# Performance work log

Hardware: AMD Instinct MI355X
Metric: run time of the kernel (lower is better)

## Reference

```python
import jax, jax.numpy as jnp
import numpy as np

B, C, H, W = 16, 256, 64, 64
K, D = 1024, 256  # codebook_dim, feature_dim (== channel)


def setup_inputs() -> dict:
    key = jax.random.key(0)
    k1, k2, k3, k4 = jax.random.split(key, 4)
    return {
        "x": jax.random.normal(k1, (B, C, H, W), dtype=jnp.float32),
        "conv_w": jax.random.normal(k2, (C, C), dtype=jnp.float32) * 0.05,
        "conv_b": jax.random.normal(k3, (C,), dtype=jnp.float32) * 0.05,
        "codebook": jax.random.normal(k4, (K, D), dtype=jnp.float32),
    }


def reference(x, conv_w, conv_b, codebook):
    # 1x1 conv: pure channel mix
    q = jnp.einsum("bchw,oc->bohw", x, conv_w) + conv_b[None, :, None, None]
    # NCHW -> NHWC -> flatten to [N, D]
    feat = jnp.transpose(q, (0, 2, 3, 1))  # [B,H,W,D]
    flat = feat.reshape(-1, D)
    # L2-normalize rows (F.normalize, eps=1e-12)
    norm = jnp.linalg.norm(flat, axis=1, keepdims=True)
    flat_n = flat / jnp.maximum(norm, 1e-12)
    d2 = (jnp.sum(flat_n * flat_n, axis=1, keepdims=True)
          - 2.0 * flat_n @ codebook.T
          + jnp.sum(codebook * codebook, axis=1)[None, :])
    idx = jnp.argmin(d2, axis=1)  # [N]
    out = codebook[idx].reshape(B, H, W, D)  # gather
    return jnp.transpose(out, (0, 3, 1, 2))  # [B,D,H,W]
```

## Files before the change

### kernel.cpp

```cpp
#include <hip/hip_runtime.h>
#include <math.h>

typedef float f4 __attribute__((ext_vector_type(4)));
typedef __attribute__((ext_vector_type(8)))  __bf16 bf16x8;
typedef __attribute__((ext_vector_type(16))) float  f32x16;
typedef __attribute__((ext_vector_type(4)))  unsigned short us4;

#define GAP_TAU 0.05f

__device__ __forceinline__ unsigned short f2bf(float f) {
    unsigned int u = __float_as_uint(f);
    return (unsigned short)((u + 0x7fffu + ((u >> 16) & 1u)) >> 16);
}

__device__ __forceinline__ float np_half128(const float* s) {
    float r[8][4];
    #pragma unroll
    for (int j = 0; j < 8; ++j)
        #pragma unroll
        for (int l = 0; l < 4; ++l) r[j][l] = s[j * 4 + l];
    #pragma unroll
    for (int m = 1; m < 4; ++m)
        #pragma unroll
        for (int j = 0; j < 8; ++j)
            #pragma unroll
            for (int l = 0; l < 4; ++l)
                r[j][l] = __fadd_rn(r[j][l], s[m * 32 + j * 4 + l]);
    float c[4];
    #pragma unroll
    for (int l = 0; l < 4; ++l) {
        float t01 = __fadd_rn(r[0][l], r[1][l]);
        float t23 = __fadd_rn(r[2][l], r[3][l]);
        float t45 = __fadd_rn(r[4][l], r[5][l]);
        float t67 = __fadd_rn(r[6][l], r[7][l]);
        c[l] = __fadd_rn(__fadd_rn(t01, t23), __fadd_rn(t45, t67));
    }
    return __fadd_rn(__fadd_rn(c[0], c[1]), __fadd_rn(c[2], c[3]));
}
__device__ __forceinline__ float np_sum256(const float* s) {
    return __fadd_rn(np_half128(s), np_half128(s + 128));
}

__global__ __launch_bounds__(256) void k_c2(const float* __restrict__ cb,
                                            float* __restrict__ c2s) {
    int k = blockIdx.x * 256 + threadIdx.x;
    if (k >= 1024) return;
    const float* row = cb + (size_t)k * 256;
    double s = 0.0;
    for (int d = 0; d < 256; ++d) { double v = (double)row[d]; s += v * v; }
    c2s[k] = (float)(s - 256.0);
}

__global__ __launch_bounds__(256) void k_pack(const float* __restrict__ cb,
                                              unsigned short* __restrict__ eh,
                                              unsigned short* __restrict__ el) {
    int i = blockIdx.x * 256 + threadIdx.x;
    float v = cb[i];
    unsigned short h = f2bf(v);
    float hf = __uint_as_float((unsigned int)h << 16);
    eh[i] = h;
    el[i] = f2bf(v - hf);
}

__global__ __launch_bounds__(256) void k_conv(const float* __restrict__ x,
                                              const float* __restrict__ w,
                                              const float* __restrict__ bias,
                                              unsigned short* __restrict__ fh,
                                              unsigned short* __restrict__ fl) {
    __shared__ f4 xs4[32 * 16];
    __shared__ f4 ws4[32 * 64];
    float* wsf = (float*)ws4;

    const int t  = threadIdx.x;
    const int og = t & 15;
    const int pg = t >> 4;
    const int b  = blockIdx.x >> 6;
    const int s0 = (blockIdx.x & 63) << 6;

    const f4* x4    = (const f4*)(x + ((size_t)b * 256) * 4096 + s0);
    const f4* w4row = (const f4*)(w + (size_t)t * 256);

    float acc[4][16];
    #pragma unroll
    for (int p = 0; p < 4; ++p)
        #pragma unroll
        for (int u = 0; u < 16; ++u) acc[p][u] = 0.f;

    for (int c0 = 0; c0 < 256; c0 += 32) {
        __syncthreads();
        #pragma unroll
        for (int j = 0; j < 2; ++j) {
            int lin = t + j * 256;
            int kk = lin >> 4, p4 = lin & 15;
            xs4[kk * 16 + p4] = x4[(size_t)(c0 + kk) * 1024 + p4];
        }
        {
            f4 wv[8];
            #pragma unroll
            for (int j = 0; j < 8; ++j) wv[j] = w4row[(c0 >> 2) + j];
            #pragma unroll
            for (int j = 0; j < 8; ++j)
                #pragma unroll
                for (int i = 0; i < 4; ++i)
                    wsf[(j * 4 + i) * 256 + t] = wv[j][i];
        }
        __syncthreads();
        #pragma unroll 8
        for (int kk = 0; kk < 32; ++kk) {
            f4 xv = xs4[kk * 16 + pg];
            f4 wv[4];
            wv[0] = ws4[kk * 64 + og];
            wv[1] = ws4[kk * 64 + og + 16];
            wv[2] = ws4[kk * 64 + og + 32];
            wv[3] = ws4[kk * 64 + og + 48];
            #pragma unroll
            for (int p = 0; p < 4; ++p)
                #pragma unroll
                for (int u = 0; u < 4; ++u)
                    #pragma unroll
                    for (int i = 0; i < 4; ++i)
                        acc[p][u * 4 + i] += xv[p] * wv[u][i];
        }
    }

    f4 bv[4];
    #pragma unroll
    for (int u = 0; u < 4; ++u) bv[u] = ((const f4*)bias)[og + 16 * u];

    const size_t n0 = (size_t)b * 4096 + s0;
    us4* fh4 = (us4*)fh;
    us4* fl4 = (us4*)fl;
    #pragma unroll
    for (int p = 0; p < 4; ++p) {
        f4 q[4];
        float n2 = 0.f;
        #pragma unroll
        for (int u = 0; u < 4; ++u)
            #pragma unroll
            for (int i = 0; i < 4; ++i) {
                float qv = acc[p][u * 4 + i] + bv[u][i];
                q[u][i] = qv;
                n2 += qv * qv;
            }
        #pragma unroll
        for (int m = 1; m <= 8; m <<= 1) n2 += __shfl_xor(n2, m, 64);
        float norm = fmaxf(sqrtf(n2), 1e-12f);
        float inv = 1.0f / norm;
        #pragma unroll
        for (int u = 0; u < 4; ++u) {
            us4 sh, sl;
            #pragma unroll
            for (int i = 0; i < 4; ++i) {
                float v = q[u][i] * inv;
                unsigned short h = f2bf(v);
                sh[i] = h;
                sl[i] = f2bf(v - __uint_as_float((unsigned int)h << 16));
            }
            size_t o8 = (n0 + pg * 4 + p) * 64 + og + 16 * u;
            fh4[o8] = sh;
            fl4[o8] = sl;
        }
    }
}

__global__ __launch_bounds__(512) void k_dist(const unsigned short* __restrict__ fh_g,
                                              const unsigned short* __restrict__ fl_g,
                                              const unsigned short* __restrict__ eh_g,
                                              const unsigned short* __restrict__ el_g,
                                              const float* __restrict__ c2s,
                                              int* __restrict__ idxout,
                                              int* __restrict__ flagcnt,
                                              int* __restrict__ flaglist) {
    __shared__ f4 fhs[64 * 32];
    __shared__ f4 fls[64 * 32];
    __shared__ float sb[8][64];
    __shared__ float sb2[8][64];
    __shared__ int   sbi[8][64];

    const int t  = threadIdx.x;
    const int w  = t >> 6;
    const int l  = t & 63;
    const int n0 = blockIdx.x * 64;

    const f4* fh4 = (const f4*)fh_g + (size_t)n0 * 32;
    const f4* fl4 = (const f4*)fl_g + (size_t)n0 * 32;
    #pragma unroll
    for (int j = 0; j < 4; ++j) {
        int lin = j * 512 + t;
        int pos = lin >> 5, c = lin & 31;
        int sw = pos * 32 + (c ^ (pos & 7));
        fhs[sw] = fh4[lin];
        fls[sw] = fl4[lin];
    }
    __syncthreads();

    f32x16 acc[4][2];
    #pragma unroll
    for (int ct = 0; ct < 4; ++ct)
        #pragma unroll
        for (int pt = 0; pt < 2; ++pt)
            #pragma unroll
            for (int r = 0; r < 16; ++r) acc[ct][pt][r] = 0.f;

    const int col = l & 31;
    const int g   = l >> 5;
    const int sw7 = col & 7;
    const f4* ehp = (const f4*)eh_g;
    const f4* elp = (const f4*)el_g;

    for (int kc = 0; kc < 16; ++kc) {
        int chunk = kc * 2 + g;
        int swc = chunk ^ sw7;
        bf16x8 ah0 = __builtin_bit_cast(bf16x8, fhs[col * 32 + swc]);
        bf16x8 al0 = __builtin_bit_cast(bf16x8, fls[col * 32 + swc]);
        bf16x8 ah1 = __builtin_bit_cast(bf16x8, fhs[(col + 32) * 32 + swc]);
        bf16x8 al1 = __builtin_bit_cast(bf16x8, fls[(col + 32) * 32 + swc]);
        #pragma unroll
        for (int ct = 0; ct < 4; ++ct) {
            int code = w * 128 + ct * 32 + col;
            bf16x8 bh = __builtin_bit_cast(bf16x8, ehp[code * 32 + chunk]);
            bf16x8 bl = __builtin_bit_cast(bf16x8, elp[code * 32 + chunk]);
            acc[ct][0] = __builtin_amdgcn_mfma_f32_32x32x16_bf16(ah0, bh, acc[ct][0], 0, 0, 0);
            acc[ct][0] = __builtin_amdgcn_mfma_f32_32x32x16_bf16(ah0, bl, acc[ct][0], 0, 0, 0);
            acc[ct][0] = __builtin_amdgcn_mfma_f32_32x32x16_bf16(al0, bh, acc[ct][0], 0, 0, 0);
            acc[ct][1] = __builtin_amdgcn_mfma_f32_32x32x16_bf16(ah1, bh, acc[ct][1], 0, 0, 0);
            acc[ct][1] = __builtin_amdgcn_mfma_f32_32x32x16_bf16(ah1, bl, acc[ct][1], 0, 0, 0);
            acc[ct][1] = __builtin_amdgcn_mfma_f32_32x32x16_bf16(al1, bh, acc[ct][1], 0, 0, 0);
        }
    }

    #pragma unroll
    for (int pt = 0; pt < 2; ++pt) {
        float best[16], best2[16]; int bidx[16];
        #pragma unroll
        for (int r = 0; r < 16; ++r) { best[r] = 3.4e38f; best2[r] = 3.4e38f; bidx[r] = 0; }
        #pragma unroll
        for (int ct = 0; ct < 4; ++ct) {
            int code = w * 128 + ct * 32 + col;
            float c2 = c2s[code];
            #pragma unroll
            for (int r = 0; r < 16; ++r) {
                float s = fmaf(-2.0f, acc[ct][pt][r], c2);
                if (s < best[r]) { best2[r] = best[r]; best[r] = s; bidx[r] = code; }
                else if (s < best2[r]) { best2[r] = s; }
            }
        }
        #pragma unroll
        for (int m = 1; m <= 16; m <<= 1) {
            #pragma unroll
            for (int r = 0; r < 16; ++r) {
                float ov  = __shfl_xor(best[r],  m, 64);
                int   oi  = __shfl_xor(bidx[r],  m, 64);
                float ov2 = __shfl_xor(best2[r], m, 64);
                bool owin = (ov < best[r]) || (ov == best[r] && oi < bidx[r]);
                float loser = owin ? best[r] : ov;
                best2[r] = fminf(fminf(best2[r], ov2), loser);
                if (owin) { best[r] = ov; bidx[r] = oi; }
            }
        }
        if (col == 0) {
            #pragma unroll
            for (int r = 0; r < 16; ++r) {
                int pos = pt * 32 + (r & 3) + 8 * (r >> 2) + 4 * g;
                sb[w][pos] = best[r]; sb2[w][pos] = best2[r]; sbi[w][pos] = bidx[r];
            }
        }
    }
    __syncthreads();

    if (t < 64) {
        float b = 3.4e38f, b2 = 3.4e38f; int bi = 0;
        #pragma unroll
        for (int ww = 0; ww < 8; ++ww) {
            float ov = sb[ww][t]; int oi = sbi[ww][t]; float ov2 = sb2[ww][t];
            bool owin = (ov < b) || (ov == b && oi < bi);
            float loser = owin ? b : ov;
            b2 = fminf(fminf(b2, ov2), loser);
            if (owin) { b = ov; bi = oi; }
        }
        int n = n0 + t;
        idxout[n] = bi;
        if (b2 - b < GAP_TAU) {
            int slot = atomicAdd(flagcnt, 1);
            if (slot < 65536) flaglist[slot] = n;
        }
    }
}

__global__ __launch_bounds__(256) void k_refine(const float* __restrict__ x,
                                                const float* __restrict__ w,
                                                const float* __restrict__ bias,
                                                const float* __restrict__ cb,
                                                const int* __restrict__ flaglist,
                                                const int* __restrict__ flagcnt,
                                                int* __restrict__ idxout) {
    __shared__ float xs[256];
    __shared__ float flat[256];
    __shared__ float fn[256];
    __shared__ float sq[256];
    __shared__ float sv[256];
    __shared__ int   si[256];
    __shared__ float bc[2];
    const int t = threadIdx.x;
    int cnt = *flagcnt;
    if (cnt > 65536) cnt = 65536;

    for (int r = blockIdx.x; r < cnt; r += gridDim.x) {
        const int n = flaglist[r];
        const int b = n >> 12, s = n & 4095;
        xs[t] = x[((size_t)b * 256 + t) * 4096 + s];
        __syncthreads();
        {
            const f4* xv4 = (const f4*)xs;
            const f4* wv4 = (const f4*)(w + (size_t)t * 256);
            float a0 = 0.f, a1 = 0.f, a2 = 0.f, a3 = 0.f;
            for (int c4 = 0; c4 < 64; ++c4) {
                f4 xv = xv4[c4];
                f4 wv = wv4[c4];
                a0 = __fadd_rn(a0, __fmul_rn(xv[0], wv[0]));
                a1 = __fadd_rn(a1, __fmul_rn(xv[1], wv[1]));
                a2 = __fadd_rn(a2, __fmul_rn(xv[2], wv[2]));
                a3 = __fadd_rn(a3, __fmul_rn(xv[3], wv[3]));
            }
            float q = __fadd_rn(__fadd_rn(a0, a1), __fadd_rn(a2, a3));
            flat[t] = __fadd_rn(q, bias[t]);
        }
        sq[t] = __fmul_rn(flat[t], flat[t]);
        __syncthreads();
        if (t == 0) bc[0] = fmaxf(__fsqrt_rn(np_sum256(sq)), 1e-12f);
        __syncthreads();
        fn[t] = __fdiv_rn(flat[t], bc[0]);
        __syncthreads();
        sq[t] = __fmul_rn(fn[t], fn[t]);
        __syncthreads();
        if (t == 0) bc[1] = np_sum256(sq);
        __syncthreads();
        const float t1f = bc[1];

        float best = 3.4e38f; int bi = 0x7fffffff;
        #pragma unroll 1
        for (int kq = 0; kq < 4; ++kq) {
            int k = kq * 256 + t;
            const f4* e4 = (const f4*)(cb + (size_t)k * 256);
            double dot = 0.0;
            float hres[2];
            #pragma unroll 1
            for (int h = 0; h < 2; ++h) {
                float rr[8][4];
                #pragma unroll
                for (int j = 0; j < 8; ++j)
                    #pragma unroll
                    for (int l = 0; l < 4; ++l) rr[j][l] = 0.f;
                #pragma unroll 1
                for (int m = 0; m < 4; ++m) {
                    #pragma unroll
                    for (int j = 0; j < 8; ++j) {
                        f4 v = e4[h * 32 + m * 8 + j];
                        #pragma unroll
                        for (int l = 0; l < 4; ++l) {
                            dot += (double)fn[h * 128 + m * 32 + j * 4 + l] * (double)v[l];
                            rr[j][l] = __fadd_rn(rr[j][l], __fmul_rn(v[l], v[l]));
                        }
                    }
                }
                float c[4];
                #pragma unroll
                for (int l = 0; l < 4; ++l) {
                    float t01 = __fadd_rn(rr[0][l], rr[1][l]);
                    float t23 = __fadd_rn(rr[2][l], rr[3][l]);
                    float t45 = __fadd_rn(rr[4][l], rr[5][l]);
                    float t67 = __fadd_rn(rr[6][l], rr[7][l]);
                    c[l] = __fadd_rn(__fadd_rn(t01, t23), __fadd_rn(t45, t67));
                }
                hres[h] = __fadd_rn(__fadd_rn(c[0], c[1]), __fadd_rn(c[2], c[3]));
            }
            float e2f = __fadd_rn(hres[0], hres[1]);
            float gf  = (float)(2.0 * dot);
            float d2  = __fadd_rn(__fsub_rn(t1f, gf), e2f);
            if (d2 < best) { best = d2; bi = k; }
        }
        sv[t] = best; si[t] = bi;
        __syncthreads();
        for (int off = 128; off > 0; off >>= 1) {
            if (t < off) {
                if (sv[t + off] < sv[t] || (sv[t + off] == sv[t] && si[t + off] < si[t])) {
                    sv[t] = sv[t + off]; si[t] = si[t + off];
                }
            }
            __syncthreads();
        }
        if (t == 0) idxout[n] = si[0];
        __syncthreads();
    }
}

__global__ __launch_bounds__(256) void k_gather(const int* __restrict__ idx,
                                                const float* __restrict__ cb,
                                                float* __restrict__ out) {
    const int t = threadIdx.x;
    const int b = blockIdx.x >> 4;
    const int s = ((blockIdx.x & 15) << 8) + t;
    const int n = b * 4096 + s;
    const int k = idx[n];
    const f4* row = (const f4*)(cb + (size_t)k * 256);
    float* ob = out + (size_t)b * 256 * 4096 + s;
    #pragma unroll 8
    for (int d4 = 0; d4 < 64; ++d4) {
        f4 v = row[d4];
        ob[(size_t)(d4 * 4 + 0) * 4096] = v[0];
        ob[(size_t)(d4 * 4 + 1) * 4096] = v[1];
        ob[(size_t)(d4 * 4 + 2) * 4096] = v[2];
        ob[(size_t)(d4 * 4 + 3) * 4096] = v[3];
    }
}

extern "C" void kernel_launch(void* const* d_in, const int* in_sizes, int n_in,
                              void* d_out, int out_size, void* d_ws, size_t ws_size,
                              hipStream_t stream) {
    const float* x    = (const float*)d_in[0];
    const float* w    = (const float*)d_in[1];
    const float* bias = (const float*)d_in[2];
    const float* cb   = (const float*)d_in[3];
    float* out = (float*)d_out;

    char* ws = (char*)d_ws;
    unsigned short* fh    = (unsigned short*)ws;
    unsigned short* fl    = (unsigned short*)(ws + 33554432);
    int*            idx   = (int*)(ws + 67108864);
    float*          c2s   = (float*)(ws + 67371008);
    int*            fcnt  = (int*)(ws + 67375104);
    int*            flist = (int*)(ws + 67375360);
    unsigned short* eh    = (unsigned short*)(ws + 67637504);
    unsigned short* el    = (unsigned short*)(ws + 68161792);

    hipMemsetAsync(fcnt, 0, 4, stream);
    k_c2    <<<4,    256, 0, stream>>>(cb, c2s);
    k_pack  <<<1024, 256, 0, stream>>>(cb, eh, el);
    k_conv  <<<1024, 256, 0, stream>>>(x, w, bias, fh, fl);
    k_dist  <<<1024, 512, 0, stream>>>(fh, fl, eh, el, c2s, idx, fcnt, flist);
    k_refine<<<256,  256, 0, stream>>>(x, w, bias, cb, flist, fcnt, idx);
    k_gather<<<256,  256, 0, stream>>>(idx, cb, out);
}
```

Baseline: 616.6 us.

## Restructure distance kernel: register-resident features, LDS-staged double-buffered codebook tiles

The distance kernel now keeps each wave's 32 feature rows (hi/lo bf16 fragments) in registers and streams the codebook through shared memory in 32-code tiles. Each tile is prefetched into registers one iteration ahead, and the argmin runs per tile instead of holding accumulators for all codes. The codebook is repacked into a chunk-major layout so tile loads coalesce, and each block now covers 256 rows, so the grid shrinks to 256 blocks. This is meant to stop every wave from re-reading codebook rows straight from global or L2 memory and to cut accumulator register pressure. In exchange it adds two barriers per tile and leaves fewer blocks to fill the GPU.

Measured after the change: 618.8 us. Within noise of the previous version (+0.4%).

```diff
diff --git a/kernel.cpp b/kernel.cpp
--- a/kernel.cpp
+++ b/kernel.cpp
@@ -55,11 +55,13 @@
                                               unsigned short* __restrict__ eh,
                                               unsigned short* __restrict__ el) {
     int i = blockIdx.x * 256 + threadIdx.x;
+    int k = i >> 8, d = i & 255;
     float v = cb[i];
     unsigned short h = f2bf(v);
     float hf = __uint_as_float((unsigned int)h << 16);
-    eh[i] = h;
-    el[i] = f2bf(v - hf);
+    int o = (((d >> 3) << 10) + k) * 8 + (d & 7);
+    eh[o] = h;
+    el[o] = f2bf(v - hf);
 }
 
 __global__ __launch_bounds__(256) void k_conv(const float* __restrict__ x,
@@ -163,126 +165,113 @@
     }
 }
 
-__global__ __launch_bounds__(512) void k_dist(const unsigned short* __restrict__ fh_g,
-                                              const unsigned short* __restrict__ fl_g,
-                                              const unsigned short* __restrict__ eh_g,
-                                              const unsigned short* __restrict__ el_g,
-                                              const float* __restrict__ c2s,
-                                              int* __restrict__ idxout,
-                                              int* __restrict__ flagcnt,
-                                              int* __restrict__ flaglist) {
-    __shared__ f4 fhs[64 * 32];
-    __shared__ f4 fls[64 * 32];
-    __shared__ float sb[8][64];
-    __shared__ float sb2[8][64];
-    __shared__ int   sbi[8][64];
-
-    const int t  = threadIdx.x;
-    const int w  = t >> 6;
-    const int l  = t & 63;
-    const int n0 = blockIdx.x * 64;
-
-    const f4* fh4 = (const f4*)fh_g + (size_t)n0 * 32;
-    const f4* fl4 = (const f4*)fl_g + (size_t)n0 * 32;
-    #pragma unroll
-    for (int j = 0; j < 4; ++j) {
-        int lin = j * 512 + t;
-        int pos = lin >> 5, c = lin & 31;
-        int sw = pos * 32 + (c ^ (pos & 7));
-        fhs[sw] = fh4[lin];
-        fls[sw] = fl4[lin];
-    }
-    __syncthreads();
-
-    f32x16 acc[4][2];
-    #pragma unroll
-    for (int ct = 0; ct < 4; ++ct)
-        #pragma unroll
-        for (int pt = 0; pt < 2; ++pt)
-            #pragma unroll
-            for (int r = 0; r < 16; ++r) acc[ct][pt][r] = 0.f;
-
+__global__ __launch_bounds__(512, 2) void k_dist(const unsigned short* __restrict__ fh_g,
+                                                 const unsigned short* __restrict__ fl_g,
+                                                 const unsigned short* __restrict__ eh_t,
+                                                 const unsigned short* __restrict__ el_t,
+                                                 const float* __restrict__ c2s,
+                                                 int* __restrict__ idxout,
+                                                 int* __restrict__ flagcnt,
+                                                 int* __restrict__ flaglist) {
+    __shared__ f4 ebuf[2048];
+
+    const int t   = threadIdx.x;
+    const int w   = t >> 6;
+    const int l   = t & 63;
     const int col = l & 31;
     const int g   = l >> 5;
-    const int sw7 = col & 7;
-    const f4* ehp = (const f4*)eh_g;
-    const f4* elp = (const f4*)el_g;
-
-    for (int kc = 0; kc < 16; ++kc) {
-        int chunk = kc * 2 + g;
-        int swc = chunk ^ sw7;
-        bf16x8 ah0 = __builtin_bit_cast(bf16x8, fhs[col * 32 + swc]);
-        bf16x8 al0 = __builtin_bit_cast(bf16x8, fls[col * 32 + swc]);
-        bf16x8 ah1 = __builtin_bit_cast(bf16x8, fhs[(col + 32) * 32 + swc]);
-        bf16x8 al1 = __builtin_bit_cast(bf16x8, fls[(col + 32) * 32 + swc]);
-        #pragma unroll
-        for (int ct = 0; ct < 4; ++ct) {
-            int code = w * 128 + ct * 32 + col;
-            bf16x8 bh = __builtin_bit_cast(bf16x8, ehp[code * 32 + chunk]);
-            bf16x8 bl = __builtin_bit_cast(bf16x8, elp[code * 32 + chunk]);
-            acc[ct][0] = __builtin_amdgcn_mfma_f32_32x32x16_bf16(ah0, bh, acc[ct][0], 0, 0, 0);
-            acc[ct][0] = __builtin_amdgcn_mfma_f32_32x32x16_bf16(ah0, bl, acc[ct][0], 0, 0, 0);
-            acc[ct][0] = __builtin_amdgcn_mfma_f32_32x32x16_bf16(al0, bh, acc[ct][0], 0, 0, 0);
-            acc[ct][1] = __builtin_amdgcn_mfma_f32_32x32x16_bf16(ah1, bh, acc[ct][1], 0, 0, 0);
-            acc[ct][1] = __builtin_amdgcn_mfma_f32_32x32x16_bf16(ah1, bl, acc[ct][1], 0, 0, 0);
-            acc[ct][1] = __builtin_amdgcn_mfma_f32_32x32x16_bf16(al1, bh, acc[ct][1], 0, 0, 0);
-        }
-    }
-
-    #pragma unroll
-    for (int pt = 0; pt < 2; ++pt) {
-        float best[16], best2[16]; int bidx[16];
-        #pragma unroll
-        for (int r = 0; r < 16; ++r) { best[r] = 3.4e38f; best2[r] = 3.4e38f; bidx[r] = 0; }
-        #pragma unroll
-        for (int ct = 0; ct < 4; ++ct) {
-            int code = w * 128 + ct * 32 + col;
-            float c2 = c2s[code];
-            #pragma unroll
-            for (int r = 0; r < 16; ++r) {
-                float s = fmaf(-2.0f, acc[ct][pt][r], c2);
-                if (s < best[r]) { best2[r] = best[r]; best[r] = s; bidx[r] = code; }
-                else if (s < best2[r]) { best2[r] = s; }
-            }
-        }
-        #pragma unroll
-        for (int m = 1; m <= 16; m <<= 1) {
-            #pragma unroll
-            for (int r = 0; r < 16; ++r) {
-                float ov  = __shfl_xor(best[r],  m, 64);
-                int   oi  = __shfl_xor(bidx[r],  m, 64);
-                float ov2 = __shfl_xor(best2[r], m, 64);
-                bool owin = (ov < best[r]) || (ov == best[r] && oi < bidx[r]);
-                float loser = owin ? best[r] : ov;
-                best2[r] = fminf(fminf(best2[r], ov2), loser);
-                if (owin) { best[r] = ov; bidx[r] = oi; }
-            }
-        }
-        if (col == 0) {
-            #pragma unroll
-            for (int r = 0; r < 16; ++r) {
-                int pos = pt * 32 + (r & 3) + 8 * (r >> 2) + 4 * g;
-                sb[w][pos] = best[r]; sb2[w][pos] = best2[r]; sbi[w][pos] = bidx[r];
-            }
-        }
-    }
-    __syncthreads();
-
-    if (t < 64) {
-        float b = 3.4e38f, b2 = 3.4e38f; int bi = 0;
-        #pragma unroll
-        for (int ww = 0; ww < 8; ++ww) {
-            float ov = sb[ww][t]; int oi = sbi[ww][t]; float ov2 = sb2[ww][t];
-            bool owin = (ov < b) || (ov == b && oi < bi);
-            float loser = owin ? b : ov;
-            b2 = fminf(fminf(b2, ov2), loser);
-            if (owin) { b = ov; bi = oi; }
-        }
-        int n = n0 + t;
-        idxout[n] = bi;
-        if (b2 - b < GAP_TAU) {
-            int slot = atomicAdd(flagcnt, 1);
-            if (slot < 65536) flaglist[slot] = n;
+    const int n0  = blockIdx.x * 256;
+    const int row = n0 + w * 32 + col;
+
+    bf16x8 ah[16], al[16];
+    {
+        const f4* fhr = (const f4*)fh_g + (size_t)row * 32;
+        const f4* flr = (const f4*)fl_g + (size_t)row * 32;
+        #pragma unroll
+        for (int s = 0; s < 16; ++s) {
+            ah[s] = __builtin_bit_cast(bf16x8, fhr[s * 2 + g]);
+            al[s] = __builtin_bit_cast(bf16x8, flr[s * 2 + g]);
+        }
+    }
+
+    const int sc0 = t & 31;
+    const int sh0 = t >> 5;
+    const f4* ehp = (const f4*)eh_t;
+    const f4* elp = (const f4*)el_t;
+
+    float best[16], best2[16]; int bidx[16];
+    #pragma unroll
+    for (int r = 0; r < 16; ++r) { best[r] = 3.4e38f; best2[r] = 3.4e38f; bidx[r] = 0; }
+
+    f4 rga[4], rgb[4];
+    rga[0] = ehp[sh0 * 1024 + sc0];
+    rga[1] = ehp[(sh0 + 16) * 1024 + sc0];
+    rga[2] = elp[sh0 * 1024 + sc0];
+    rga[3] = elp[(sh0 + 16) * 1024 + sc0];
+
+    for (int ct = 0; ct < 32; ++ct) {
+        const f4* cur = (ct & 1) ? rgb : rga;
+        f4*       nxt = (ct & 1) ? rga : rgb;
+        __syncthreads();
+        ebuf[t]         = cur[0];
+        ebuf[t + 512]   = cur[1];
+        ebuf[t + 1024]  = cur[2];
+        ebuf[t + 1536]  = cur[3];
+        if (ct + 1 < 32) {
+            int kb = (ct + 1) * 32;
+            nxt[0] = ehp[sh0 * 1024 + kb + sc0];
+            nxt[1] = ehp[(sh0 + 16) * 1024 + kb + sc0];
+            nxt[2] = elp[sh0 * 1024 + kb + sc0];
+            nxt[3] = elp[(sh0 + 16) * 1024 + kb + sc0];
+        }
+        __syncthreads();
+
+        f32x16 acc;
+        #pragma unroll
+        for (int r = 0; r < 16; ++r) acc[r] = 0.f;
+        #pragma unroll
+        for (int s = 0; s < 16; ++s) {
+            int chunk = s * 2 + g;
+            bf16x8 bh = __builtin_bit_cast(bf16x8, ebuf[chunk * 32 + col]);
+            bf16x8 bl = __builtin_bit_cast(bf16x8, ebuf[1024 + chunk * 32 + col]);
+            acc = __builtin_amdgcn_mfma_f32_32x32x16_bf16(ah[s], bh, acc, 0, 0, 0);
+            acc = __builtin_amdgcn_mfma_f32_32x32x16_bf16(ah[s], bl, acc, 0, 0, 0);
+            acc = __builtin_amdgcn_mfma_f32_32x32x16_bf16(al[s], bh, acc, 0, 0, 0);
+        }
+
+        const int code = ct * 32 + col;
+        const float c2 = c2s[code];
+        #pragma unroll
+        for (int r = 0; r < 16; ++r) {
+            float sc = fmaf(-2.0f, acc[r], c2);
+            if (sc < best[r]) { best2[r] = best[r]; best[r] = sc; bidx[r] = code; }
+            else if (sc < best2[r]) { best2[r] = sc; }
+        }
+    }
+
+    #pragma unroll
+    for (int m = 1; m <= 16; m <<= 1) {
+        #pragma unroll
+        for (int r = 0; r < 16; ++r) {
+            float ov  = __shfl_xor(best[r],  m, 64);
+            int   oi  = __shfl_xor(bidx[r],  m, 64);
+            float ov2 = __shfl_xor(best2[r], m, 64);
+            bool owin = (ov < best[r]) || (ov == best[r] && oi < bidx[r]);
+            float loser = owin ? best[r] : ov;
+            best2[r] = fminf(fminf(best2[r], ov2), loser);
+            if (owin) { best[r] = ov; bidx[r] = oi; }
+        }
+    }
+    if (col == 0) {
+        #pragma unroll
+        for (int r = 0; r < 16; ++r) {
+            int pos = (r & 3) + 8 * (r >> 2) + 4 * g;
+            int n = n0 + w * 32 + pos;
+            idxout[n] = bidx[r];
+            if (best2[r] - best[r] < GAP_TAU) {
+                int slot = atomicAdd(flagcnt, 1);
+                if (slot < 65536) flaglist[slot] = n;
+            }
         }
     }
 }
@@ -437,7 +426,7 @@
     k_c2    <<<4,    256, 0, stream>>>(cb, c2s);
     k_pack  <<<1024, 256, 0, stream>>>(cb, eh, el);
     k_conv  <<<1024, 256, 0, stream>>>(x, w, bias, fh, fl);
-    k_dist  <<<1024, 512, 0, stream>>>(fh, fl, eh, el, c2s, idx, fcnt, flist);
+    k_dist  <<<256,  512, 0, stream>>>(fh, fl, eh, el, c2s, idx, fcnt, flist);
     k_refine<<<256,  256, 0, stream>>>(x, w, bias, cb, flist, fcnt, idx);
     k_gather<<<256,  256, 0, stream>>>(idx, cb, out);
 }
```
